# Optimization experiments

Measured on AMD Instinct MI355X. Metric: run time of the kernel, lower is better.

Reference implementation:

```python
import jax, jax.numpy as jnp
import numpy as np

B, S, E, H, D = 2, 2048, 1024, 16, 64  # batch, seq(=max_seq_len), embed_dim, heads, atten_dim


def setup_inputs() -> dict:
    key = jax.random.key(0)
    ks = jax.random.split(key, 9)
    s = 0.02
    return {
        "x": jax.random.normal(ks[0], (B, S, E), jnp.float32),
        "Wq": jax.random.normal(ks[1], (H, E, D), jnp.float32) * s,
        "Wk": jax.random.normal(ks[2], (H, E, D), jnp.float32) * s,
        "Wv": jax.random.normal(ks[3], (H, E, D), jnp.float32) * s,
        "bq": jax.random.normal(ks[4], (H, D), jnp.float32) * s,
        "bk": jax.random.normal(ks[5], (H, D), jnp.float32) * s,
        "bv": jax.random.normal(ks[6], (H, D), jnp.float32) * s,
        "Wp": jax.random.normal(ks[7], (H * D, E), jnp.float32) * s,
        "bp": jax.random.normal(ks[8], (E,), jnp.float32) * s,
    }


def reference(x, Wq, Wk, Wv, bq, bk, bv, Wp, bp):
    scale = jnp.sqrt(jnp.float32(D))
    # per-head projections, all heads at once: [B,H,S,D]
    q = jnp.einsum("bse,hed->bhsd", x, Wq) + bq[:, None, :]
    k = jnp.einsum("bse,hed->bhsd", x, Wk) + bk[:, None, :]
    v = jnp.einsum("bse,hed->bhsd", x, Wv) + bv[:, None, :]
    # causal scores [B,H,S,S], additive -inf mask above diagonal (as in the buffer)
    score = jnp.einsum("bhsd,bhtd->bhst", q, k) / scale
    mask = jnp.triu(jnp.full((S, S), -jnp.inf, jnp.float32), k=1)
    score = score + mask
    probs = jax.nn.softmax(score, axis=-1)
    attn = jnp.einsum("bhst,bhtd->bhsd", probs, v)
    # concat heads -> [B,S,H*D], then projection + ReLU
    concat = attn.transpose(0, 2, 1, 3).reshape(B, S, H * D)
    out = jax.nn.relu(concat @ Wp + bp)
    return out
```

## Files before the change

### kernel.cpp

```cpp
#include <hip/hip_runtime.h>

#define S_LEN 2048
#define E_DIM 1024
#define H_NUM 16
#define D_DIM 64

typedef unsigned short u16;
using bf16x8 = __attribute__((ext_vector_type(8))) short;
using f32x4  = __attribute__((ext_vector_type(4))) float;

#define MFMA16(A, B, C) __builtin_amdgcn_mfma_f32_16x16x32_bf16(A, B, C, 0, 0, 0)
#define QSCALE 0.18033688011112042f

__device__ __forceinline__ u16 f2bf(float f) {
    unsigned u = __float_as_uint(f);
    u += 0x7fffu + ((u >> 16) & 1u);
    return (u16)(u >> 16);
}
__device__ __forceinline__ f32x4 fzero4() { f32x4 z; z[0]=0.f; z[1]=0.f; z[2]=0.f; z[3]=0.f; return z; }

__device__ __forceinline__ unsigned cvtpk(float a, float b) {
    unsigned r;
    asm("v_cvt_pk_bf16_f32 %0, %1, %2" : "=v"(r) : "v"(a), "v"(b));
    return r;
}
__device__ __forceinline__ float fexp2(float x) {
#if __has_builtin(__builtin_amdgcn_exp2f)
    return __builtin_amdgcn_exp2f(x);
#else
    float r; asm("v_exp_f32 %0, %1" : "=v"(r) : "v"(x)); return r;
#endif
}
__device__ __forceinline__ float frcp(float x) {
#if __has_builtin(__builtin_amdgcn_rcpf)
    return __builtin_amdgcn_rcpf(x);
#else
    float r; asm("v_rcp_f32 %0, %1" : "=v"(r) : "v"(x)); return r;
#endif
}

__device__ __forceinline__ void gll16(const u16* g, u16* l) {
    __builtin_amdgcn_global_load_lds(
        (const __attribute__((address_space(1))) void*)g,
        (__attribute__((address_space(3))) void*)l, 16, 0, 0);
}

__device__ __forceinline__ void stage64(const u16* __restrict__ g, int gstride,
                                        u16* l, int wave, int lane) {
    #pragma unroll
    for (int i = 0; i < 2; i++) {
        const int r  = wave * 16 + i * 8 + (lane >> 3);
        const int sl = (lane & 7) ^ (r & 7);
        gll16(g + (size_t)r * gstride + sl * 8, l + (wave * 16 + i * 8) * 64);
    }
}
__device__ __forceinline__ bf16x8 ldswz(const u16* t, int rr, int hh, int quad) {
    const int sl = ((hh << 2) + quad) ^ (rr & 7);
    return *(const bf16x8*)(t + rr * 64 + sl * 8);
}

__device__ __forceinline__ void cvt_t_tile(const float* __restrict__ bin, u16* __restrict__ bout,
                                           int R, int C, int r0, int c0) {
    __shared__ float t[64][65];
    const int tid = threadIdx.x;
    const int lr = tid >> 2, lc = (tid & 3) * 16;

    const float* src = bin + (size_t)(r0 + lr) * C + c0 + lc;
    #pragma unroll
    for (int j = 0; j < 4; j++) {
        float4 f = *(const float4*)(src + j * 4);
        t[lr][lc + j * 4 + 0] = f.x; t[lr][lc + j * 4 + 1] = f.y;
        t[lr][lc + j * 4 + 2] = f.z; t[lr][lc + j * 4 + 3] = f.w;
    }
    __syncthreads();

    u16* dst = bout + (size_t)(c0 + lr) * R + r0 + lc;
    u16 vals[16];
    #pragma unroll
    for (int i = 0; i < 16; i++) vals[i] = f2bf(t[lc + i][lr]);
    uint4 pa, pb;
    pa.x = vals[0] | (vals[1] << 16);  pa.y = vals[2] | (vals[3] << 16);
    pa.z = vals[4] | (vals[5] << 16);  pa.w = vals[6] | (vals[7] << 16);
    pb.x = vals[8] | (vals[9] << 16);  pb.y = vals[10] | (vals[11] << 16);
    pb.z = vals[12] | (vals[13] << 16); pb.w = vals[14] | (vals[15] << 16);
    *(uint4*)dst = pa;
    *(uint4*)(dst + 8) = pb;
}

__global__ __launch_bounds__(256) void cvt_all(
    const float* __restrict__ x, u16* __restrict__ xb, int n,
    const float* __restrict__ Wq, const float* __restrict__ Wk, const float* __restrict__ Wv,
    u16* __restrict__ wqt, u16* __restrict__ wkt, u16* __restrict__ wvt,
    const float* __restrict__ Wp, u16* __restrict__ wpt)
{
    const int bid = blockIdx.x;
    if (bid < 4096) {
        int i4 = (bid * 256 + threadIdx.x) * 4;
        if (i4 < n) {
            float4 f = *(const float4*)(x + i4);
            unsigned lo = (unsigned)f2bf(f.x) | ((unsigned)f2bf(f.y) << 16);
            unsigned hi = (unsigned)f2bf(f.z) | ((unsigned)f2bf(f.w) << 16);
            uint2 p; p.x = lo; p.y = hi;
            *(uint2*)(xb + i4) = p;
        }
    } else if (bid < 4096 + 768) {
        const int t  = bid - 4096;
        const int z  = t >> 4;
        const int ry = t & 15;
        const int which = z >> 4, bh = z & 15;
        const float* in = (which == 0) ? Wq : (which == 1) ? Wk : Wv;
        u16* outp = (which == 0) ? wqt : (which == 1) ? wkt : wvt;
        cvt_t_tile(in + (size_t)bh * E_DIM * D_DIM, outp + (size_t)bh * E_DIM * D_DIM,
                   E_DIM, D_DIM, ry * 64, 0);
    } else {
        const int t = bid - (4096 + 768);
        cvt_t_tile(Wp, wpt, H_NUM * D_DIM, E_DIM, (t >> 4) * 64, (t & 15) * 64);
    }
}

__global__ __launch_bounds__(256) void qkv_gemm(
    const u16* __restrict__ xb, const u16* __restrict__ wcat,
    const float* __restrict__ bq, const float* __restrict__ bk, const float* __restrict__ bv,
    u16* __restrict__ oq, u16* __restrict__ okk, u16* __restrict__ ov)
{
    const int bid = blockIdx.x;
    const int sw  = (bid & 7) * 96 + (bid >> 3);
    const int m0  = (sw & 31) * 128;
    const int n0  = (sw >> 5) * 128;

    __shared__ u16 As[128 * 64];
    __shared__ u16 Bs[128 * 64];

    const int tid  = threadIdx.x;
    const int wave = tid >> 6, lane = tid & 63, quad = lane >> 4, l16 = lane & 15;
    const int mh = wave >> 1, nh = wave & 1;

    f32x4 acc[4][4];
    #pragma unroll
    for (int j = 0; j < 4; j++)
        #pragma unroll
        for (int mi = 0; mi < 4; mi++) acc[j][mi] = fzero4();

    for (int k0 = 0; k0 < E_DIM; k0 += 64) {
        __syncthreads();
        #pragma unroll
        for (int i = 0; i < 4; i++) {
            const int r  = wave * 32 + i * 8 + (lane >> 3);
            const int sl = (lane & 7) ^ (r & 7);
            gll16(xb   + (size_t)(m0 + r) * E_DIM + k0 + sl * 8, &As[(wave * 32 + i * 8) * 64]);
            gll16(wcat + (size_t)(n0 + r) * E_DIM + k0 + sl * 8, &Bs[(wave * 32 + i * 8) * 64]);
        }
        __syncthreads();

        #pragma unroll
        for (int kq = 0; kq < 2; kq++) {
            bf16x8 af[4];
            #pragma unroll
            for (int mi = 0; mi < 4; mi++) {
                const int rr = mh * 64 + mi * 16 + l16;
                af[mi] = *(const bf16x8*)(&As[rr * 64 + (((kq << 2) + quad) ^ (rr & 7)) * 8]);
            }
            #pragma unroll
            for (int j = 0; j < 4; j++) {
                const int rr = nh * 64 + j * 16 + l16;
                bf16x8 bfv = *(const bf16x8*)(&Bs[rr * 64 + (((kq << 2) + quad) ^ (rr & 7)) * 8]);
                #pragma unroll
                for (int mi = 0; mi < 4; mi++)
                    acc[j][mi] = MFMA16(af[mi], bfv, acc[j][mi]);
            }
        }
    }

    const int t = n0 >> 10;
    if (t < 2) {
        const float scl = (t == 0) ? QSCALE : 1.0f;
        const float* bias = (t == 0) ? bq : bk;
        u16* dst = (t == 0) ? oq : okk;
        #pragma unroll
        for (int j = 0; j < 4; j++) {
            const int n = n0 + nh * 64 + j * 16 + l16;
            const int h = (n >> 6) & 15, d = n & 63;
            float bia = bias[h * D_DIM + d];
            #pragma unroll
            for (int mi = 0; mi < 4; mi++) {
                #pragma unroll
                for (int r = 0; r < 4; r++) {
                    int m = m0 + mh * 64 + mi * 16 + quad * 4 + r;
                    int b = m >> 11, s = m & 2047;
                    dst[((size_t)(b * H_NUM + h) * S_LEN + s) * D_DIM + d] =
                        f2bf((acc[j][mi][r] + bia) * scl);
                }
            }
        }
    } else {
        const int b  = m0 >> 11, s0 = m0 & 2047;
        const int h0 = (n0 >> 6) & 15;
        u16* Tb0 = As;
        u16* Tb1 = Bs;
        #pragma unroll
        for (int pass = 0; pass < 2; ++pass) {
            __syncthreads();
            if (mh == pass) {
                u16* Tb = nh ? Tb1 : Tb0;
                #pragma unroll
                for (int j = 0; j < 4; j++) {
                    const int n = n0 + nh * 64 + j * 16 + l16;
                    const int d = n & 63, hh = (n >> 6) & 15;
                    const float bia = bv[hh * D_DIM + d];
                    const int nl = j * 16 + l16;
                    #pragma unroll
                    for (int mi = 0; mi < 4; mi++) {
                        uint2 pk;
                        pk.x = cvtpk(acc[j][mi][0] + bia, acc[j][mi][1] + bia);
                        pk.y = cvtpk(acc[j][mi][2] + bia, acc[j][mi][3] + bia);
                        *(uint2*)(&Tb[nl * 72 + mi * 16 + quad * 4]) = pk;
                    }
                }
            }
            __syncthreads();
            #pragma unroll
            for (int g = 0; g < 4; ++g) {
                const int rowi = g * 32 + (tid >> 3);
                const int ml = (tid & 7) * 8;
                const u16* srcp = (rowi < 64 ? Tb0 : Tb1) + (rowi & 63) * 72 + ml;
                const int hh = h0 + (rowi >> 6), d = rowi & 63;
                u16* dstp = ov + ((size_t)(b * H_NUM + hh) * D_DIM + d) * S_LEN
                               + s0 + pass * 64 + ml;
                *(uint4*)dstp = *(const uint4*)srcp;
            }
        }
    }
}

__global__ __launch_bounds__(256, 2) void attn_fwd(
    const u16* __restrict__ q, const u16* __restrict__ k, const u16* __restrict__ vt,
    u16* __restrict__ concat)
{
    const int bid  = blockIdx.x;
    const int halfg = bid >> 8;
    const int pi   = (bid & 255) >> 5;
    const int p    = halfg ? (15 - pi) : pi;
    const int g    = bid & 31;
    const int h    = g & 15;
    const int bb   = g >> 4;
    const int qa = p, qb = 31 - p;

    const size_t headoff = (size_t)(bb * H_NUM + h) * S_LEN * D_DIM;
    const u16* qh  = q  + headoff;
    const u16* kh  = k  + headoff;
    const u16* vth = vt + headoff;

    __shared__ u16 QaL[64 * 64];
    __shared__ u16 QbL[64 * 64];
    __shared__ u16 Ks[2][64 * 64];
    __shared__ u16 Vts[2][64 * 64];
    __shared__ u16 Psa[4][16 * 72];
    __shared__ u16 Psb[4][16 * 72];

    const int tid  = threadIdx.x;
    const int wave = tid >> 6, lane = tid & 63, quad = lane >> 4, l16 = lane & 15;

    stage64(qh + (size_t)qa * 64 * D_DIM, D_DIM, QaL,    wave, lane);
    stage64(qh + (size_t)qb * 64 * D_DIM, D_DIM, QbL,    wave, lane);
    stage64(kh,                           D_DIM, Ks[0],  wave, lane);
    stage64(vth,                          S_LEN, Vts[0], wave, lane);
    __syncthreads();

    bf16x8 bqa0 = ldswz(QaL, wave * 16 + l16, 0, quad);
    bf16x8 bqa1 = ldswz(QaL, wave * 16 + l16, 1, quad);
    bf16x8 bqb0 = ldswz(QbL, wave * 16 + l16, 0, quad);
    bf16x8 bqb1 = ldswz(QbL, wave * 16 + l16, 1, quad);

    f32x4 oa[4], ob[4];
    #pragma unroll
    for (int nt = 0; nt < 4; nt++) { oa[nt] = fzero4(); ob[nt] = fzero4(); }
    float la = 0.f, lb = 0.f;

    const int qga = qa * 64 + wave * 16 + l16;
    const int qgb = qb * 64 + wave * 16 + l16;

    u16* pwa = &Psa[wave][0];
    u16* pwb = &Psb[wave][0];

    for (int kt = 0; kt <= qb; kt++) {
        __syncthreads();
        if (kt < qb) {
            stage64(kh + (size_t)(kt + 1) * 64 * D_DIM, D_DIM, Ks[(kt + 1) & 1],  wave, lane);
            stage64(vth + (kt + 1) * 64,                S_LEN, Vts[(kt + 1) & 1], wave, lane);
        }
        const u16* Kc = Ks[kt & 1];
        const u16* Vc = Vts[kt & 1];
        const bool both = (kt <= qa);

        f32x4 stb[4], sta[4];
        __builtin_amdgcn_s_setprio(1);
        #pragma unroll
        for (int nt = 0; nt < 4; nt++) {
            const int rr = nt * 16 + l16;
            bf16x8 ak0 = ldswz(Kc, rr, 0, quad);
            bf16x8 ak1 = ldswz(Kc, rr, 1, quad);
            stb[nt] = MFMA16(ak0, bqb0, fzero4());
            stb[nt] = MFMA16(ak1, bqb1, stb[nt]);
            if (both) {
                sta[nt] = MFMA16(ak0, bqa0, fzero4());
                sta[nt] = MFMA16(ak1, bqa1, sta[nt]);
            }
        }
        __builtin_amdgcn_s_setprio(0);

        bf16x8 bv0[4], bv1[4];
        #pragma unroll
        for (int nt = 0; nt < 4; nt++) {
            bv0[nt] = ldswz(Vc, nt * 16 + l16, 0, quad);
            bv1[nt] = ldswz(Vc, nt * 16 + l16, 1, quad);
        }

        #pragma unroll
        for (int nt = 0; nt < 4; nt++) {
            float pe[4];
            if (kt == qb) {
                #pragma unroll
                for (int r = 0; r < 4; r++) {
                    int kkg = kt * 64 + nt * 16 + quad * 4 + r;
                    pe[r] = (kkg > qgb) ? 0.f : fexp2(stb[nt][r]);
                }
            } else {
                #pragma unroll
                for (int r = 0; r < 4; r++) pe[r] = fexp2(stb[nt][r]);
            }
            lb += (pe[0] + pe[1]) + (pe[2] + pe[3]);
            uint2 pk;
            pk.x = cvtpk(pe[0], pe[1]);
            pk.y = cvtpk(pe[2], pe[3]);
            *(uint2*)(&pwb[l16 * 72 + nt * 16 + quad * 4]) = pk;
        }
        if (both) {
            #pragma unroll
            for (int nt = 0; nt < 4; nt++) {
                float pe[4];
                if (kt == qa) {
                    #pragma unroll
                    for (int r = 0; r < 4; r++) {
                        int kkg = kt * 64 + nt * 16 + quad * 4 + r;
                        pe[r] = (kkg > qga) ? 0.f : fexp2(sta[nt][r]);
                    }
                } else {
                    #pragma unroll
                    for (int r = 0; r < 4; r++) pe[r] = fexp2(sta[nt][r]);
                }
                la += (pe[0] + pe[1]) + (pe[2] + pe[3]);
                uint2 pk;
                pk.x = cvtpk(pe[0], pe[1]);
                pk.y = cvtpk(pe[2], pe[3]);
                *(uint2*)(&pwa[l16 * 72 + nt * 16 + quad * 4]) = pk;
            }
        }

        {
            bf16x8 ap0 = *(const bf16x8*)(&pwb[l16 * 72 + quad * 8]);
            bf16x8 ap1 = *(const bf16x8*)(&pwb[l16 * 72 + 32 + quad * 8]);
            __builtin_amdgcn_s_setprio(1);
            #pragma unroll
            for (int nt = 0; nt < 4; nt++) {
                ob[nt] = MFMA16(ap0, bv0[nt], ob[nt]);
                ob[nt] = MFMA16(ap1, bv1[nt], ob[nt]);
            }
            __builtin_amdgcn_s_setprio(0);
        }
        if (both) {
            bf16x8 ap0 = *(const bf16x8*)(&pwa[l16 * 72 + quad * 8]);
            bf16x8 ap1 = *(const bf16x8*)(&pwa[l16 * 72 + 32 + quad * 8]);
            __builtin_amdgcn_s_setprio(1);
            #pragma unroll
            for (int nt = 0; nt < 4; nt++) {
                oa[nt] = MFMA16(ap0, bv0[nt], oa[nt]);
                oa[nt] = MFMA16(ap1, bv1[nt], oa[nt]);
            }
            __builtin_amdgcn_s_setprio(0);
        }
    }

    lb += __shfl_xor(lb, 16); lb += __shfl_xor(lb, 32);
    la += __shfl_xor(la, 16); la += __shfl_xor(la, 32);

    #pragma unroll
    for (int r = 0; r < 4; r++) {
        const int srcl = quad * 4 + r;
        float lbi = frcp(__shfl(lb, srcl));
        float lai = frcp(__shfl(la, srcl));
        int sqa = qa * 64 + wave * 16 + quad * 4 + r;
        int sqb = qb * 64 + wave * 16 + quad * 4 + r;
        #pragma unroll
        for (int nt = 0; nt < 4; nt++) {
            concat[((size_t)(bb * S_LEN + sqa)) * E_DIM + h * D_DIM + nt * 16 + l16] =
                f2bf(oa[nt][r] * lai);
            concat[((size_t)(bb * S_LEN + sqb)) * E_DIM + h * D_DIM + nt * 16 + l16] =
                f2bf(ob[nt][r] * lbi);
        }
    }
}

__global__ __launch_bounds__(256, 2) void out_proj(
    const u16* __restrict__ concat, const u16* __restrict__ wpt,
    const float* __restrict__ bp, float* __restrict__ out)
{
    const int bid = blockIdx.x;
    const int mt  = (bid & 7) * 8 + ((bid >> 3) & 7);
    const int nt0 = bid >> 6;
    const int m0 = mt * 64;
    const int n0 = nt0 * 128;

    __shared__ u16 As[2][64 * 64];
    __shared__ u16 Bs[2][128 * 64];

    const int tid  = threadIdx.x;
    const int wave = tid >> 6, lane = tid & 63, quad = lane >> 4, l16 = lane & 15;
    const int mh = wave >> 1, nh = wave & 1;

    f32x4 acc[4][2];
    #pragma unroll
    for (int j = 0; j < 4; j++)
        #pragma unroll
        for (int mi = 0; mi < 2; mi++) acc[j][mi] = fzero4();

    stage64(concat + (size_t)m0 * E_DIM, E_DIM, As[0], wave, lane);
    stage64(wpt + (size_t)n0 * E_DIM,        E_DIM, Bs[0],           wave, lane);
    stage64(wpt + (size_t)(n0 + 64) * E_DIM, E_DIM, Bs[0] + 64 * 64, wave, lane);

    for (int kt = 0; kt < 16; kt++) {
        __syncthreads();
        if (kt < 15) {
            const int k0 = (kt + 1) * 64;
            u16* an = As[(kt + 1) & 1];
            u16* bn = Bs[(kt + 1) & 1];
            stage64(concat + (size_t)m0 * E_DIM + k0, E_DIM, an, wave, lane);
            stage64(wpt + (size_t)n0 * E_DIM + k0,        E_DIM, bn,           wave, lane);
            stage64(wpt + (size_t)(n0 + 64) * E_DIM + k0, E_DIM, bn + 64 * 64, wave, lane);
        }
        const u16* Ac = As[kt & 1];
        const u16* Bc = Bs[kt & 1];

        #pragma unroll
        for (int kq = 0; kq < 2; kq++) {
            bf16x8 af[2];
            #pragma unroll
            for (int mi = 0; mi < 2; mi++)
                af[mi] = ldswz(Ac, mh * 32 + mi * 16 + l16, kq, quad);
            __builtin_amdgcn_s_setprio(1);
            #pragma unroll
            for (int j = 0; j < 4; j++) {
                bf16x8 bfv = ldswz(Bc, nh * 64 + j * 16 + l16, kq, quad);
                #pragma unroll
                for (int mi = 0; mi < 2; mi++)
                    acc[j][mi] = MFMA16(af[mi], bfv, acc[j][mi]);
            }
            __builtin_amdgcn_s_setprio(0);
        }
    }

    #pragma unroll
    for (int j = 0; j < 4; j++) {
        int n = n0 + nh * 64 + j * 16 + l16;
        float bia = bp[n];
        #pragma unroll
        for (int mi = 0; mi < 2; mi++) {
            #pragma unroll
            for (int r = 0; r < 4; r++) {
                int m = m0 + mh * 32 + mi * 16 + quad * 4 + r;
                out[(size_t)m * E_DIM + n] = fmaxf(acc[j][mi][r] + bia, 0.f);
            }
        }
    }
}

extern "C" void kernel_launch(void* const* d_in, const int* in_sizes, int n_in,
                              void* d_out, int out_size, void* d_ws, size_t ws_size,
                              hipStream_t stream)
{
    (void)in_sizes; (void)n_in; (void)out_size; (void)ws_size;
    const float* x  = (const float*)d_in[0];
    const float* Wq = (const float*)d_in[1];
    const float* Wk = (const float*)d_in[2];
    const float* Wv = (const float*)d_in[3];
    const float* bq = (const float*)d_in[4];
    const float* bk = (const float*)d_in[5];
    const float* bv = (const float*)d_in[6];
    const float* Wp = (const float*)d_in[7];
    const float* bp = (const float*)d_in[8];
    float* out = (float*)d_out;

    const size_t QKV_ELEMS = (size_t)2 * H_NUM * S_LEN * D_DIM;
    const size_t W_ELEMS   = (size_t)H_NUM * E_DIM * D_DIM;

    u16* q   = (u16*)d_ws;
    u16* k   = q   + QKV_ELEMS;
    u16* v   = k   + QKV_ELEMS;
    u16* cc  = v   + QKV_ELEMS;
    u16* xb  = cc  + QKV_ELEMS;
    u16* wqt = xb  + QKV_ELEMS;
    u16* wkt = wqt + W_ELEMS;
    u16* wvt = wkt + W_ELEMS;
    u16* wpt = wvt + W_ELEMS;

    cvt_all<<<dim3(4096 + 768 + 256), 256, 0, stream>>>(
        x, xb, (int)QKV_ELEMS, Wq, Wk, Wv, wqt, wkt, wvt, Wp, wpt);

    qkv_gemm<<<dim3(768), 256, 0, stream>>>(xb, wqt, bq, bk, bv, q, k, v);
    attn_fwd<<<dim3(512), 256, 0, stream>>>(q, k, v, cc);
    out_proj<<<dim3(512), 256, 0, stream>>>(cc, wpt, bp, out);
}
```

Measured before the change: 182.9 us.

## Double-buffer LDS tiles in QKV GEMM and prefetch the next K-slice

The QKV projection GEMM now keeps two LDS buffers for the A and B tiles. While the current 64-wide K-slice is fed to MFMA, it issues the global-to-LDS loads for the next slice, so each iteration needs only one barrier instead of two. The kernel also switches to a plain 2D grid without the previous block swizzle and adds a min-2-blocks occupancy hint. Doubling LDS use may limit occupancy, and dropping the swizzle may hurt L2 locality.

```diff
diff --git a/kernel.cpp b/kernel.cpp
--- a/kernel.cpp
+++ b/kernel.cpp
@@ -118,22 +118,21 @@
     }
 }
 
-__global__ __launch_bounds__(256) void qkv_gemm(
+__global__ __launch_bounds__(256, 2) void qkv_gemm(
     const u16* __restrict__ xb, const u16* __restrict__ wcat,
     const float* __restrict__ bq, const float* __restrict__ bk, const float* __restrict__ bv,
     u16* __restrict__ oq, u16* __restrict__ okk, u16* __restrict__ ov)
 {
-    const int bid = blockIdx.x;
-    const int sw  = (bid & 7) * 96 + (bid >> 3);
-    const int m0  = (sw & 31) * 128;
-    const int n0  = (sw >> 5) * 128;
-
-    __shared__ u16 As[128 * 64];
-    __shared__ u16 Bs[128 * 64];
+    const int m0 = blockIdx.x * 128;
+    const int n0 = blockIdx.y * 128;
+
+    __shared__ u16 As[2][128 * 64];
+    __shared__ u16 Bs[2][128 * 64];
 
     const int tid  = threadIdx.x;
     const int wave = tid >> 6, lane = tid & 63, quad = lane >> 4, l16 = lane & 15;
     const int mh = wave >> 1, nh = wave & 1;
+    const int sr = lane >> 3, sl = lane & 7;
 
     f32x4 acc[4][4];
     #pragma unroll
@@ -141,16 +140,29 @@
         #pragma unroll
         for (int mi = 0; mi < 4; mi++) acc[j][mi] = fzero4();
 
-    for (int k0 = 0; k0 < E_DIM; k0 += 64) {
+    #pragma unroll
+    for (int i = 0; i < 4; i++) {
+        const int r  = wave * 32 + i * 8 + sr;
+        const int sx = sl ^ (r & 7);
+        gll16(xb   + (size_t)(m0 + r) * E_DIM + sx * 8, &As[0][(wave * 32 + i * 8) * 64]);
+        gll16(wcat + (size_t)(n0 + r) * E_DIM + sx * 8, &Bs[0][(wave * 32 + i * 8) * 64]);
+    }
+
+    for (int kt = 0; kt < 16; kt++) {
         __syncthreads();
-        #pragma unroll
-        for (int i = 0; i < 4; i++) {
-            const int r  = wave * 32 + i * 8 + (lane >> 3);
-            const int sl = (lane & 7) ^ (r & 7);
-            gll16(xb   + (size_t)(m0 + r) * E_DIM + k0 + sl * 8, &As[(wave * 32 + i * 8) * 64]);
-            gll16(wcat + (size_t)(n0 + r) * E_DIM + k0 + sl * 8, &Bs[(wave * 32 + i * 8) * 64]);
-        }
-        __syncthreads();
+        if (kt < 15) {
+            const int k0 = (kt + 1) * 64;
+            const int bn = (kt + 1) & 1;
+            #pragma unroll
+            for (int i = 0; i < 4; i++) {
+                const int r  = wave * 32 + i * 8 + sr;
+                const int sx = sl ^ (r & 7);
+                gll16(xb   + (size_t)(m0 + r) * E_DIM + k0 + sx * 8, &As[bn][(wave * 32 + i * 8) * 64]);
+                gll16(wcat + (size_t)(n0 + r) * E_DIM + k0 + sx * 8, &Bs[bn][(wave * 32 + i * 8) * 64]);
+            }
+        }
+        const u16* Ac = As[kt & 1];
+        const u16* Bc = Bs[kt & 1];
 
         #pragma unroll
         for (int kq = 0; kq < 2; kq++) {
@@ -158,12 +170,12 @@
             #pragma unroll
             for (int mi = 0; mi < 4; mi++) {
                 const int rr = mh * 64 + mi * 16 + l16;
-                af[mi] = *(const bf16x8*)(&As[rr * 64 + (((kq << 2) + quad) ^ (rr & 7)) * 8]);
+                af[mi] = *(const bf16x8*)(&Ac[rr * 64 + (((kq << 2) + quad) ^ (rr & 7)) * 8]);
             }
             #pragma unroll
             for (int j = 0; j < 4; j++) {
                 const int rr = nh * 64 + j * 16 + l16;
-                bf16x8 bfv = *(const bf16x8*)(&Bs[rr * 64 + (((kq << 2) + quad) ^ (rr & 7)) * 8]);
+                bf16x8 bfv = *(const bf16x8*)(&Bc[rr * 64 + (((kq << 2) + quad) ^ (rr & 7)) * 8]);
                 #pragma unroll
                 for (int mi = 0; mi < 4; mi++)
                     acc[j][mi] = MFMA16(af[mi], bfv, acc[j][mi]);
@@ -195,8 +207,8 @@
     } else {
         const int b  = m0 >> 11, s0 = m0 & 2047;
         const int h0 = (n0 >> 6) & 15;
-        u16* Tb0 = As;
-        u16* Tb1 = Bs;
+        u16* Tb0 = As[0];
+        u16* Tb1 = Bs[0];
         #pragma unroll
         for (int pass = 0; pass < 2; ++pass) {
             __syncthreads();
@@ -505,7 +517,7 @@
     cvt_all<<<dim3(4096 + 768 + 256), 256, 0, stream>>>(
         x, xb, (int)QKV_ELEMS, Wq, Wk, Wv, wqt, wkt, wvt, Wp, wpt);
 
-    qkv_gemm<<<dim3(768), 256, 0, stream>>>(xb, wqt, bq, bk, bv, q, k, v);
+    qkv_gemm<<<dim3(32, 24), 256, 0, stream>>>(xb, wqt, bq, bk, bv, q, k, v);
     attn_fwd<<<dim3(512), 256, 0, stream>>>(q, k, v, cc);
     out_proj<<<dim3(512), 256, 0, stream>>>(cc, wpt, bp, out);
 }
```

After: 179.4 us. No clear change (-1.9%).

## Double-buffer B tiles and load A fragments directly from global in QKV GEMM

Applied to the files above, without the earlier changes.

The QKV projection GEMM now double-buffers the weight tile in LDS and loads the activation fragments straight from global memory into registers, prefetching the next k-step while computing the current one. It also raises MFMA wave priority, sets launch_bounds to 2 blocks, and replaces the swizzled 1D block mapping with a plain 2D grid. The goal is to hide global load latency behind MFMA work and drop the A-side LDS round trip. In exchange it uses more registers, and the A loads from global may coalesce less well. Dropping the swizzle may also hurt L2 reuse.

```diff
diff --git a/kernel.cpp b/kernel.cpp
--- a/kernel.cpp
+++ b/kernel.cpp
@@ -118,22 +118,25 @@
     }
 }
 
-__global__ __launch_bounds__(256) void qkv_gemm(
+__global__ __launch_bounds__(256, 2) void qkv_gemm(
     const u16* __restrict__ xb, const u16* __restrict__ wcat,
     const float* __restrict__ bq, const float* __restrict__ bk, const float* __restrict__ bv,
     u16* __restrict__ oq, u16* __restrict__ okk, u16* __restrict__ ov)
 {
-    const int bid = blockIdx.x;
-    const int sw  = (bid & 7) * 96 + (bid >> 3);
-    const int m0  = (sw & 31) * 128;
-    const int n0  = (sw >> 5) * 128;
-
-    __shared__ u16 As[128 * 64];
-    __shared__ u16 Bs[128 * 64];
+    const int m0 = blockIdx.x * 128;
+    const int n0 = blockIdx.y * 128;
+
+    __shared__ u16 Bs[2][128 * 64];
 
     const int tid  = threadIdx.x;
     const int wave = tid >> 6, lane = tid & 63, quad = lane >> 4, l16 = lane & 15;
     const int mh = wave >> 1, nh = wave & 1;
+    const int sr = lane >> 3, sl8 = lane & 7;
+
+    const u16* aptr0 = xb + (size_t)(m0 + mh * 64 + l16) * E_DIM + quad * 8;
+    const u16* aptr1 = aptr0 + 16 * E_DIM;
+    const u16* aptr2 = aptr0 + 32 * E_DIM;
+    const u16* aptr3 = aptr0 + 48 * E_DIM;
 
     f32x4 acc[4][4];
     #pragma unroll
@@ -141,35 +144,66 @@
         #pragma unroll
         for (int mi = 0; mi < 4; mi++) acc[j][mi] = fzero4();
 
-    for (int k0 = 0; k0 < E_DIM; k0 += 64) {
+#define STAGE_B(K0, BUF)                                                              \
+    _Pragma("unroll")                                                                 \
+    for (int i = 0; i < 4; i++) {                                                     \
+        const int r  = wave * 32 + i * 8 + sr;                                        \
+        const int sx = sl8 ^ (r & 7);                                                 \
+        gll16(wcat + (size_t)(n0 + r) * E_DIM + (K0) + sx * 8,                        \
+              &Bs[BUF][(wave * 32 + i * 8) * 64]);                                    \
+    }
+
+#define LOAD_A(DST, K0)                                                               \
+    _Pragma("unroll")                                                                 \
+    for (int kq = 0; kq < 2; kq++) {                                                  \
+        DST[kq][0] = *(const bf16x8*)(aptr0 + (K0) + kq * 32);                        \
+        DST[kq][1] = *(const bf16x8*)(aptr1 + (K0) + kq * 32);                        \
+        DST[kq][2] = *(const bf16x8*)(aptr2 + (K0) + kq * 32);                        \
+        DST[kq][3] = *(const bf16x8*)(aptr3 + (K0) + kq * 32);                        \
+    }
+
+#define COMPUTE(AF, BUF)                                                              \
+    _Pragma("unroll")                                                                 \
+    for (int kq = 0; kq < 2; kq++) {                                                  \
+        __builtin_amdgcn_s_setprio(1);                                                \
+        _Pragma("unroll")                                                             \
+        for (int j = 0; j < 4; j++) {                                                 \
+            const int rr = nh * 64 + j * 16 + l16;                                    \
+            bf16x8 bfv = *(const bf16x8*)(&Bs[BUF][rr * 64 +                          \
+                              (((kq << 2) + quad) ^ (rr & 7)) * 8]);                  \
+            _Pragma("unroll")                                                         \
+            for (int mi = 0; mi < 4; mi++)                                            \
+                acc[j][mi] = MFMA16(AF[kq][mi], bfv, acc[j][mi]);                     \
+        }                                                                             \
+        __builtin_amdgcn_s_setprio(0);                                                \
+    }
+
+    bf16x8 afA[2][4], afB[2][4];
+
+    STAGE_B(0, 0);
+    LOAD_A(afA, 0);
+
+    #pragma unroll
+    for (int kt2 = 0; kt2 < 8; kt2++) {
         __syncthreads();
-        #pragma unroll
-        for (int i = 0; i < 4; i++) {
-            const int r  = wave * 32 + i * 8 + (lane >> 3);
-            const int sl = (lane & 7) ^ (r & 7);
-            gll16(xb   + (size_t)(m0 + r) * E_DIM + k0 + sl * 8, &As[(wave * 32 + i * 8) * 64]);
-            gll16(wcat + (size_t)(n0 + r) * E_DIM + k0 + sl * 8, &Bs[(wave * 32 + i * 8) * 64]);
-        }
+        {
+            const int kn = kt2 * 128 + 64;
+            STAGE_B(kn, 1);
+            LOAD_A(afB, kn);
+        }
+        COMPUTE(afA, 0);
+
         __syncthreads();
-
-        #pragma unroll
-        for (int kq = 0; kq < 2; kq++) {
-            bf16x8 af[4];
-            #pragma unroll
-            for (int mi = 0; mi < 4; mi++) {
-                const int rr = mh * 64 + mi * 16 + l16;
-                af[mi] = *(const bf16x8*)(&As[rr * 64 + (((kq << 2) + quad) ^ (rr & 7)) * 8]);
-            }
-            #pragma unroll
-            for (int j = 0; j < 4; j++) {
-                const int rr = nh * 64 + j * 16 + l16;
-                bf16x8 bfv = *(const bf16x8*)(&Bs[rr * 64 + (((kq << 2) + quad) ^ (rr & 7)) * 8]);
-                #pragma unroll
-                for (int mi = 0; mi < 4; mi++)
-                    acc[j][mi] = MFMA16(af[mi], bfv, acc[j][mi]);
-            }
-        }
-    }
+        if (kt2 < 7) {
+            const int kn = kt2 * 128 + 128;
+            STAGE_B(kn, 0);
+            LOAD_A(afA, kn);
+        }
+        COMPUTE(afB, 1);
+    }
+#undef STAGE_B
+#undef LOAD_A
+#undef COMPUTE
 
     const int t = n0 >> 10;
     if (t < 2) {
@@ -195,8 +229,8 @@
     } else {
         const int b  = m0 >> 11, s0 = m0 & 2047;
         const int h0 = (n0 >> 6) & 15;
-        u16* Tb0 = As;
-        u16* Tb1 = Bs;
+        u16* Tb0 = Bs[0];
+        u16* Tb1 = Bs[1];
         #pragma unroll
         for (int pass = 0; pass < 2; ++pass) {
             __syncthreads();
@@ -505,7 +539,7 @@
     cvt_all<<<dim3(4096 + 768 + 256), 256, 0, stream>>>(
         x, xb, (int)QKV_ELEMS, Wq, Wk, Wv, wqt, wkt, wvt, Wp, wpt);
 
-    qkv_gemm<<<dim3(768), 256, 0, stream>>>(xb, wqt, bq, bk, bv, q, k, v);
+    qkv_gemm<<<dim3(32, 24), 256, 0, stream>>>(xb, wqt, bq, bk, bv, q, k, v);
     attn_fwd<<<dim3(512), 256, 0, stream>>>(q, k, v, cc);
     out_proj<<<dim3(512), 256, 0, stream>>>(cc, wpt, bp, out);
 }
```

Result: slower. 197.4 us (+7.9%).

## Double-buffer QKV GEMM LDS with two-wave 64x128 tiles and raised MFMA priority

Applied to the files above, without the earlier changes.

Rewrites qkv_gemm to use 128-thread blocks in which each wave computes a 64x128 output tile. The K loop now runs in steps of 32, and LDS is double-buffered so the next tile's global-to-LDS loads are issued before computing the current one, leaving one barrier per iteration. s_setprio is raised around the MFMA section, and the bid swizzle is replaced by a plain 2D grid. The goals are to hide load latency and cut barrier overhead. In exchange, per-wave register pressure is higher (32 accumulators) and L2 locality may be lost without the swizzle.

```diff
diff --git a/kernel.cpp b/kernel.cpp
--- a/kernel.cpp
+++ b/kernel.cpp
@@ -118,58 +118,77 @@
     }
 }
 
-__global__ __launch_bounds__(256) void qkv_gemm(
+__global__ __launch_bounds__(128, 2) void qkv_gemm(
     const u16* __restrict__ xb, const u16* __restrict__ wcat,
     const float* __restrict__ bq, const float* __restrict__ bk, const float* __restrict__ bv,
     u16* __restrict__ oq, u16* __restrict__ okk, u16* __restrict__ ov)
 {
-    const int bid = blockIdx.x;
-    const int sw  = (bid & 7) * 96 + (bid >> 3);
-    const int m0  = (sw & 31) * 128;
-    const int n0  = (sw >> 5) * 128;
-
-    __shared__ u16 As[128 * 64];
-    __shared__ u16 Bs[128 * 64];
+    const int m0 = blockIdx.x * 128;
+    const int n0 = blockIdx.y * 128;
+
+    __shared__ u16 As[2][64 * 64];
+    __shared__ u16 Bs[2][64 * 64];
 
     const int tid  = threadIdx.x;
     const int wave = tid >> 6, lane = tid & 63, quad = lane >> 4, l16 = lane & 15;
-    const int mh = wave >> 1, nh = wave & 1;
-
-    f32x4 acc[4][4];
-    #pragma unroll
-    for (int j = 0; j < 4; j++)
+
+    f32x4 acc[8][4];
+    #pragma unroll
+    for (int j = 0; j < 8; j++)
         #pragma unroll
         for (int mi = 0; mi < 4; mi++) acc[j][mi] = fzero4();
 
-    for (int k0 = 0; k0 < E_DIM; k0 += 64) {
+#define STAGE(K0, BUF)                                                               \
+    _Pragma("unroll")                                                                \
+    for (int i = 0; i < 2; i++) {                                                    \
+        const int r  = wave * 32 + i * 8 + (lane >> 3);           \
+        const int s  = (lane & 7) ^ (r & 7);                      \
+        const int mr = r + ((s >> 2) << 6);                      \
+        const int kc = (s & 3) * 8;                              \
+        gll16(xb   + (size_t)(m0 + mr) * E_DIM + (K0) + kc,                          \
+              &As[BUF][(wave * 32 + i * 8) * 64]);                                   \
+        gll16(wcat + (size_t)(n0 + mr) * E_DIM + (K0) + kc,                          \
+              &Bs[BUF][(wave * 32 + i * 8) * 64]);                                   \
+        const int r2  = wave * 32 + 16 + i * 8 + (lane >> 3);                        \
+        const int s2  = (lane & 7) ^ (r2 & 7);                                       \
+        const int mr2 = r2 + ((s2 >> 2) << 6);                                       \
+        const int kc2 = (s2 & 3) * 8;                                                \
+        gll16(xb   + (size_t)(m0 + mr2) * E_DIM + (K0) + kc2,                        \
+              &As[BUF][(wave * 32 + 16 + i * 8) * 64]);                              \
+        gll16(wcat + (size_t)(n0 + mr2) * E_DIM + (K0) + kc2,                        \
+              &Bs[BUF][(wave * 32 + 16 + i * 8) * 64]);                              \
+    }
+
+    STAGE(0, 0);
+
+    for (int kt = 0; kt < 32; kt++) {
         __syncthreads();
-        #pragma unroll
-        for (int i = 0; i < 4; i++) {
-            const int r  = wave * 32 + i * 8 + (lane >> 3);
-            const int sl = (lane & 7) ^ (r & 7);
-            gll16(xb   + (size_t)(m0 + r) * E_DIM + k0 + sl * 8, &As[(wave * 32 + i * 8) * 64]);
-            gll16(wcat + (size_t)(n0 + r) * E_DIM + k0 + sl * 8, &Bs[(wave * 32 + i * 8) * 64]);
-        }
-        __syncthreads();
-
-        #pragma unroll
-        for (int kq = 0; kq < 2; kq++) {
-            bf16x8 af[4];
-            #pragma unroll
-            for (int mi = 0; mi < 4; mi++) {
-                const int rr = mh * 64 + mi * 16 + l16;
-                af[mi] = *(const bf16x8*)(&As[rr * 64 + (((kq << 2) + quad) ^ (rr & 7)) * 8]);
-            }
-            #pragma unroll
-            for (int j = 0; j < 4; j++) {
-                const int rr = nh * 64 + j * 16 + l16;
-                bf16x8 bfv = *(const bf16x8*)(&Bs[rr * 64 + (((kq << 2) + quad) ^ (rr & 7)) * 8]);
-                #pragma unroll
-                for (int mi = 0; mi < 4; mi++)
-                    acc[j][mi] = MFMA16(af[mi], bfv, acc[j][mi]);
-            }
-        }
-    }
+        if (kt < 31) {
+            const int kn = (kt + 1) * 32;
+            if ((kt & 1) == 0) { STAGE(kn, 1); } else { STAGE(kn, 0); }
+        }
+        const u16* Ac = As[kt & 1];
+        const u16* Bc = Bs[kt & 1];
+
+        bf16x8 af[4];
+        #pragma unroll
+        for (int mi = 0; mi < 4; mi++) {
+            const int row = mi * 16 + l16;
+            af[mi] = *(const bf16x8*)(&Ac[row * 64 + ((((wave << 2) + quad)) ^ (row & 7)) * 8]);
+        }
+        __builtin_amdgcn_s_setprio(1);
+        #pragma unroll
+        for (int j = 0; j < 8; j++) {
+            const int row = (j & 3) * 16 + l16;
+            bf16x8 bfv = *(const bf16x8*)(&Bc[row * 64 +
+                              ((((j >> 2) << 2) + quad) ^ (row & 7)) * 8]);
+            #pragma unroll
+            for (int mi = 0; mi < 4; mi++)
+                acc[j][mi] = MFMA16(af[mi], bfv, acc[j][mi]);
+        }
+        __builtin_amdgcn_s_setprio(0);
+    }
+#undef STAGE
 
     const int t = n0 >> 10;
     if (t < 2) {
@@ -177,15 +196,15 @@
         const float* bias = (t == 0) ? bq : bk;
         u16* dst = (t == 0) ? oq : okk;
         #pragma unroll
-        for (int j = 0; j < 4; j++) {
-            const int n = n0 + nh * 64 + j * 16 + l16;
+        for (int j = 0; j < 8; j++) {
+            const int n = n0 + j * 16 + l16;
             const int h = (n >> 6) & 15, d = n & 63;
             float bia = bias[h * D_DIM + d];
             #pragma unroll
             for (int mi = 0; mi < 4; mi++) {
                 #pragma unroll
                 for (int r = 0; r < 4; r++) {
-                    int m = m0 + mh * 64 + mi * 16 + quad * 4 + r;
+                    int m = m0 + wave * 64 + mi * 16 + quad * 4 + r;
                     int b = m >> 11, s = m & 2047;
                     dst[((size_t)(b * H_NUM + h) * S_LEN + s) * D_DIM + d] =
                         f2bf((acc[j][mi][r] + bia) * scl);
@@ -195,19 +214,19 @@
     } else {
         const int b  = m0 >> 11, s0 = m0 & 2047;
         const int h0 = (n0 >> 6) & 15;
-        u16* Tb0 = As;
-        u16* Tb1 = Bs;
+        u16* Tb0 = &As[0][0];
+        u16* Tb1 = &Bs[0][0];
         #pragma unroll
         for (int pass = 0; pass < 2; ++pass) {
             __syncthreads();
-            if (mh == pass) {
-                u16* Tb = nh ? Tb1 : Tb0;
+            if (wave == pass) {
                 #pragma unroll
-                for (int j = 0; j < 4; j++) {
-                    const int n = n0 + nh * 64 + j * 16 + l16;
+                for (int j = 0; j < 8; j++) {
+                    const int n = n0 + j * 16 + l16;
                     const int d = n & 63, hh = (n >> 6) & 15;
                     const float bia = bv[hh * D_DIM + d];
-                    const int nl = j * 16 + l16;
+                    u16* Tb = (j < 4) ? Tb0 : Tb1;
+                    const int nl = (j & 3) * 16 + l16;
                     #pragma unroll
                     for (int mi = 0; mi < 4; mi++) {
                         uint2 pk;
@@ -219,8 +238,8 @@
             }
             __syncthreads();
             #pragma unroll
-            for (int g = 0; g < 4; ++g) {
-                const int rowi = g * 32 + (tid >> 3);
+            for (int g = 0; g < 8; ++g) {
+                const int rowi = g * 16 + (tid >> 3);
                 const int ml = (tid & 7) * 8;
                 const u16* srcp = (rowi < 64 ? Tb0 : Tb1) + (rowi & 63) * 72 + ml;
                 const int hh = h0 + (rowi >> 6), d = rowi & 63;
@@ -505,7 +524,7 @@
     cvt_all<<<dim3(4096 + 768 + 256), 256, 0, stream>>>(
         x, xb, (int)QKV_ELEMS, Wq, Wk, Wv, wqt, wkt, wvt, Wp, wpt);
 
-    qkv_gemm<<<dim3(768), 256, 0, stream>>>(xb, wqt, bq, bk, bv, q, k, v);
+    qkv_gemm<<<dim3(32, 24), 128, 0, stream>>>(xb, wqt, bq, bk, bv, q, k, v);
     attn_fwd<<<dim3(512), 256, 0, stream>>>(q, k, v, cc);
     out_proj<<<dim3(512), 256, 0, stream>>>(cc, wpt, bp, out);
 }
```

New measurement: 175.3 us. 1.04x faster.
